# Optimization experiments

Hardware: AMD Instinct MI355X
Metric: run time of the kernel (lower is better)

## Reference

```python
import jax, jax.numpy as jnp
import numpy as np

B, N, D, K = 32, 4096, 128, 512
NPB = 2048          # unique tail nodes per batch (>= K so topk branch is taken)
M = B * NPB         # total unique tail nodes
E = B * N           # total edges
NUM_ENT = 10000


def setup_inputs() -> dict:
    key = jax.random.key(0)
    ks = jax.random.split(key, 18)
    f = lambda k, s: jax.random.normal(k, s, dtype=jnp.float32)
    inp = {
        "q_head": f(ks[0], (B, D)),
        "q_rel": f(ks[1], (B, D)),
        "q_time": f(ks[2], (B, D)),
        "r_neighbor": f(ks[3], (B, N, D)),
        "t_neighbor": f(ks[4], (B, N, D)),
        "time_neighbor": f(ks[5], (B, N, D)),
        "hidden": f(ks[6], (E, D)),
        "tail_emd": jnp.zeros((M, D), jnp.float32),  # scatter out-buffer
    }
    # tail_index: each edge of batch b scatters into that batch's node slab
    local = jax.random.randint(ks[7], (B, N), 0, NPB)
    inp["tail_index"] = (local + jnp.arange(B)[:, None] * NPB).reshape(E).astype(jnp.int32)
    # tail_nodes: [M,3] = (batch id, tail entity, time)
    batch_col = jnp.repeat(jnp.arange(B), NPB)
    tail_col = jax.random.randint(ks[8], (M,), 0, NUM_ENT)
    time_col = jax.random.randint(ks[9], (M,), 0, 365)
    inp["tail_nodes"] = jnp.stack([batch_col, tail_col, time_col], axis=-1).astype(jnp.int32)
    # linear-layer params (torch nn.Linear-style scaling)
    s3, s1 = 1.0 / np.sqrt(3 * D), 1.0 / np.sqrt(D)
    inp["W_q"] = f(ks[10], (3 * D, D)) * s3
    inp["b_q"] = jnp.zeros((D,), jnp.float32)
    inp["W_a"] = f(ks[11], (3 * D, D)) * s3
    inp["b_a"] = jnp.zeros((D,), jnp.float32)
    inp["W_att"] = f(ks[12], (3 * D, 1)) * s3
    inp["b_att"] = jnp.zeros((1,), jnp.float32)
    inp["W_rule"] = f(ks[13], (D, 1)) * s1
    inp["b_rule"] = jnp.zeros((1,), jnp.float32)
    inp["W_out"] = f(ks[14], (D, D)) * s1
    inp["b_out"] = jnp.zeros((D,), jnp.float32)
    return inp


def reference(q_head, q_rel, q_time, r_neighbor, t_neighbor, time_neighbor,
              hidden, tail_emd, tail_index, tail_nodes,
              W_q, b_q, W_a, b_a, W_att, b_att, W_rule, b_rule, W_out, b_out):
    # act = identity (module default). reduce = 'sum'.
    # raw message per edge: [E, D]
    message = (q_head[:, None, :] + r_neighbor + time_neighbor).reshape(E, D)
    # query / neighbor projections
    query = jnp.concatenate([q_head, q_rel, q_time], axis=-1) @ W_q + b_q      # [B, D]
    neigh = jnp.concatenate([r_neighbor, t_neighbor, time_neighbor], -1) @ W_a + b_a  # [B, N, D]
    q = query[:, None, :]
    qa = jnp.concatenate([q * neigh, q - neigh, q + neigh], axis=-1)           # [B, N, 3D]
    att1 = jax.nn.sigmoid(qa @ W_att + b_att).reshape(E, 1)
    att2 = jax.nn.sigmoid(hidden @ W_rule + b_rule)                            # [E, 1]
    att = (att1 + att2) * 0.5
    msg = att * message
    # scatter-sum aggregation over unique tail nodes
    seg = lambda v: jax.ops.segment_sum(v, tail_index, num_segments=M)
    tail_agg = tail_emd + seg(msg)            # scatter(..., out=tail_emd)
    new_hidden = seg(hidden)                  # [M, D]
    agg_att = seg(att[:, 0])                  # [M]
    # per-batch top-k over aggregated attention (each batch has NPB >= K nodes)
    nodes_batch = tail_nodes[:, 0]
    scores = jnp.where(nodes_batch[None, :] == jnp.arange(B)[:, None],
                       agg_att[None, :], -jnp.inf)                             # [B, M]
    _, idx = jax.lax.top_k(scores, K)                                          # [B, K] global node ids
    new_nodes = jnp.stack([tail_nodes[:, 1][idx], tail_nodes[:, 2][idx]], -1)  # [B, K, 2]
    emd = tail_agg[idx]                                                        # [B, K, D]
    hid = new_hidden[idx]                                                      # [B, K, D]
    out_emd = emd @ W_out + b_out                                              # act=identity
    return new_nodes, out_emd, hid
```

## Files before the change

### kernel.cpp

```cpp
#include <hip/hip_runtime.h>
#include <math.h>

#define B 32
#define N 4096
#define D 128
#define KTOP 512
#define NPB 2048
#define MSEG (B * NPB)
#define E (B * N)
#define MAXC 32

__global__ __launch_bounds__(128) void k0_precompute(
    const float* __restrict__ qh, const float* __restrict__ qr,
    const float* __restrict__ qt, const float* __restrict__ Wq,
    const float* __restrict__ bq, const float* __restrict__ Wa,
    const float* __restrict__ ba, const float* __restrict__ Watt,
    const float* __restrict__ batt, double* __restrict__ vws,
    double* __restrict__ c2ws, float* __restrict__ vf,
    float* __restrict__ c2f) {
  int b = blockIdx.x, d = threadIdx.x;
  __shared__ double u[128];
  __shared__ double red[128];
  const float* qhb = qh + b * 128;
  const float* qrb = qr + b * 128;
  const float* qtb = qt + b * 128;
  double acc = (double)bq[d];
  for (int i = 0; i < 128; ++i) acc += (double)qhb[i] * (double)Wq[i * 128 + d];
  for (int i = 0; i < 128; ++i) acc += (double)qrb[i] * (double)Wq[(128 + i) * 128 + d];
  for (int i = 0; i < 128; ++i) acc += (double)qtb[i] * (double)Wq[(256 + i) * 128 + d];
  double w1 = (double)Watt[d], w2 = (double)Watt[128 + d], w3 = (double)Watt[256 + d];
  double ud = acc * w1 - w2 + w3;
  u[d] = ud;
  red[d] = acc * (w2 + w3) + (double)ba[d] * ud;
  __syncthreads();
  for (int s = 64; s > 0; s >>= 1) {
    if (d < s) red[d] += red[d + s];
    __syncthreads();
  }
  if (d == 0) {
    double c2 = red[0] + (double)batt[0];
    c2ws[b] = c2;
    c2f[b] = (float)c2;
  }
  for (int i = d; i < 384; i += 128) {
    double vv = 0.0;
    for (int dd = 0; dd < 128; ++dd) vv += (double)Wa[i * 128 + dd] * u[dd];
    vws[b * 384 + i] = vv;
    vf[b * 384 + i] = (float)vv;
  }
}

__global__ __launch_bounds__(256) void k1_att(
    const float* __restrict__ r, const float* __restrict__ t,
    const float* __restrict__ tm, const float* __restrict__ hidden,
    const float* __restrict__ Wrule, const float* __restrict__ brule,
    const float* __restrict__ vf, const float* __restrict__ c2f,
    float* __restrict__ attw) {
  int tid = threadIdx.x;
  int h = tid >> 5;
  int l = tid & 31;
  int base = blockIdx.x * 64;
  int b = base >> 12;
  const float4* vb = (const float4*)(vf + b * 384);
  float4 v0 = vb[l];
  float4 v1 = vb[32 + l];
  float4 v2 = vb[64 + l];
  float4 wr = ((const float4*)Wrule)[l];
  float c2 = c2f[b];
  float br = brule[0];
#pragma unroll 4
  for (int i = 0; i < 8; ++i) {
    int e = base + i * 8 + h;
    size_t eo = (size_t)e * 128 + l * 4;
    float4 ra = *(const float4*)(r + eo);
    float4 ta = *(const float4*)(t + eo);
    float4 ma = *(const float4*)(tm + eo);
    float4 ha = *(const float4*)(hidden + eo);
    float p1 = ra.x * v0.x + ra.y * v0.y + ra.z * v0.z + ra.w * v0.w;
    p1 += ta.x * v1.x + ta.y * v1.y + ta.z * v1.z + ta.w * v1.w;
    p1 += ma.x * v2.x + ma.y * v2.y + ma.z * v2.z + ma.w * v2.w;
    float p2 = ha.x * wr.x + ha.y * wr.y + ha.z * wr.z + ha.w * wr.w;
#pragma unroll
    for (int off = 16; off > 0; off >>= 1) {
      p1 += __shfl_xor(p1, off);
      p2 += __shfl_xor(p2, off);
    }
    if (l == 0) {
      float a1 = 1.0f / (1.0f + expf(-(p1 + c2)));
      float a2 = 1.0f / (1.0f + expf(-(p2 + br)));
      attw[e] = 0.5f * (a1 + a2);
    }
  }
}

__global__ __launch_bounds__(256) void kb_build(const int* __restrict__ tidx,
                                                int* __restrict__ counts,
                                                int* __restrict__ lists) {
  int e = blockIdx.x * 256 + threadIdx.x;
  int m = tidx[e];
  int pos = atomicAdd(&counts[m], 1);
  if (pos < MAXC) lists[m * MAXC + pos] = e;
}

__global__ __launch_bounds__(256) void k_agg(const int* __restrict__ counts,
                                             const int* __restrict__ lists,
                                             const float* __restrict__ attw,
                                             float* __restrict__ agg_att) {
  int m = blockIdx.x * 256 + threadIdx.x;
  int cnt = counts[m];
  if (cnt > MAXC) cnt = MAXC;
  float s = 0.f;
  for (int j = 0; j < cnt; ++j) s += attw[lists[m * MAXC + j]];
  agg_att[m] = s;
}

__global__ __launch_bounds__(256) void k6_topk(
    const float* __restrict__ agg_att, const int* __restrict__ tail_nodes,
    float* __restrict__ out_nodes, int* __restrict__ idxw) {
  __shared__ float sv[2048];
  int b = blockIdx.x >> 3;
  int chunk = blockIdx.x & 7;
  int tid = threadIdx.x;
  for (int s = tid; s < 2048; s += 256) sv[s] = agg_att[b * 2048 + s];
  __syncthreads();
  int i = chunk * 256 + tid;
  float vi = sv[i];
  int rank = 0;
#pragma unroll 8
  for (int j = 0; j < 2048; ++j) {
    float vj = sv[j];
    rank += (vj > vi) || (vj == vi && j < i);
  }
  if (rank < KTOP) {
    int gm = b * 2048 + i;
    int p = b * KTOP + rank;
    out_nodes[p * 2 + 0] = (float)tail_nodes[gm * 3 + 1];
    out_nodes[p * 2 + 1] = (float)tail_nodes[gm * 3 + 2];
    idxw[p] = gm;
  }
}

__global__ __launch_bounds__(256) void k7_out(
    const float* __restrict__ tail_emd, const float* __restrict__ r,
    const float* __restrict__ tm, const float* __restrict__ hidden,
    const float* __restrict__ qh, const float* __restrict__ attw,
    const int* __restrict__ counts, const int* __restrict__ lists,
    const float* __restrict__ Wout, const float* __restrict__ bout,
    const int* __restrict__ idxw, float* __restrict__ out_emd,
    float* __restrict__ out_hid) {
  __shared__ float Ws[16384];
  __shared__ float es[256];
  int tid = threadIdx.x;
  int sub = tid >> 7, d = tid & 127;
  for (int i = tid; i < 16384; i += 256) Ws[i] = Wout[i];
  int base = blockIdx.x * 32;
  float bo = bout[d];
  for (int j = 0; j < 32; j += 2) {
    int row = base + j + sub;
    int m = idxw[row];
    int b = m >> 11;
    int cnt = counts[m];
    if (cnt > MAXC) cnt = MAXC;
    float accT = tail_emd[(size_t)m * 128 + d];
    float accH = 0.f;
    float qhd = qh[b * 128 + d];
    for (int jj = 0; jj < cnt; ++jj) {
      int e = lists[m * MAXC + jj];
      float a = attw[e];
      size_t eo = (size_t)e * 128 + d;
      accT += a * (qhd + r[eo] + tm[eo]);
      accH += hidden[eo];
    }
    __syncthreads();
    es[sub * 128 + d] = accT;
    __syncthreads();
    float acc = bo;
#pragma unroll 8
    for (int i = 0; i < 128; ++i) acc += es[sub * 128 + i] * Ws[i * 128 + d];
    out_emd[(size_t)row * 128 + d] = acc;
    out_hid[(size_t)row * 128 + d] = accH;
  }
}

extern "C" void kernel_launch(void* const* d_in, const int* in_sizes, int n_in,
                              void* d_out, int out_size, void* d_ws,
                              size_t ws_size, hipStream_t stream) {
  const float* q_head = (const float*)d_in[0];
  const float* q_rel = (const float*)d_in[1];
  const float* q_time = (const float*)d_in[2];
  const float* r_nb = (const float*)d_in[3];
  const float* t_nb = (const float*)d_in[4];
  const float* tm_nb = (const float*)d_in[5];
  const float* hidden = (const float*)d_in[6];
  const float* tail_emd = (const float*)d_in[7];
  const int* tail_index = (const int*)d_in[8];
  const int* tail_nodes = (const int*)d_in[9];
  const float* W_q = (const float*)d_in[10];
  const float* b_q = (const float*)d_in[11];
  const float* W_a = (const float*)d_in[12];
  const float* b_a = (const float*)d_in[13];
  const float* W_att = (const float*)d_in[14];
  const float* b_att = (const float*)d_in[15];
  const float* W_rule = (const float*)d_in[16];
  const float* b_rule = (const float*)d_in[17];
  const float* W_out = (const float*)d_in[18];
  const float* b_out = (const float*)d_in[19];

  char* ws = (char*)d_ws;
  double* vws = (double*)(ws + 0);
  double* c2ws = (double*)(ws + 98304);
  float* vf = (float*)(ws + 98560);
  float* c2f = (float*)(ws + 147712);
  float* attw = (float*)(ws + 147968);
  int* counts = (int*)(ws + 672256);
  int* lists = (int*)(ws + 934400);
  float* agg_att = (float*)(ws + 9323008);
  int* idxw = (int*)(ws + 9585152);

  float* out_nodes = (float*)d_out;
  float* out_emd = (float*)d_out + (size_t)B * KTOP * 2;
  float* out_hid = out_emd + (size_t)B * KTOP * 128;

  hipMemsetAsync(counts, 0, MSEG * sizeof(int), stream);
  k0_precompute<<<B, 128, 0, stream>>>(q_head, q_rel, q_time, W_q, b_q, W_a,
                                       b_a, W_att, b_att, vws, c2ws, vf, c2f);
  k1_att<<<E / 64, 256, 0, stream>>>(r_nb, t_nb, tm_nb, hidden, W_rule, b_rule,
                                     vf, c2f, attw);
  kb_build<<<E / 256, 256, 0, stream>>>(tail_index, counts, lists);
  k_agg<<<MSEG / 256, 256, 0, stream>>>(counts, lists, attw, agg_att);
  k6_topk<<<B * 8, 256, 0, stream>>>(agg_att, tail_nodes, out_nodes, idxw);
  k7_out<<<(B * KTOP) / 32, 256, 0, stream>>>(tail_emd, r_nb, tm_nb, hidden,
                                              q_head, attw, counts, lists,
                                              W_out, b_out, idxw, out_emd,
                                              out_hid);
}
```

Before: 501.3 us.

## Fuse attention aggregation into att kernel and restructure output projection

Attention aggregation moves into the attention kernel as double-precision atomics, which removes the separate aggregation kernel; top-k now ranks on doubles. The output kernel stops staging the full W_out in shared memory, handles 16 rows per block, and does a register-blocked float4 matmul after gathering rows, giving more blocks. The precompute kernel splits its serial double accumulations into four chains and drops unused double outputs. The trade-offs are atomic contention, an extra memset, and a double-width shared array in top-k.

```diff
diff --git a/kernel.cpp b/kernel.cpp
--- a/kernel.cpp
+++ b/kernel.cpp
@@ -9,14 +9,14 @@
 #define MSEG (B * NPB)
 #define E (B * N)
 #define MAXC 32
+#define K7ROWS 16
 
 __global__ __launch_bounds__(128) void k0_precompute(
     const float* __restrict__ qh, const float* __restrict__ qr,
     const float* __restrict__ qt, const float* __restrict__ Wq,
     const float* __restrict__ bq, const float* __restrict__ Wa,
     const float* __restrict__ ba, const float* __restrict__ Watt,
-    const float* __restrict__ batt, double* __restrict__ vws,
-    double* __restrict__ c2ws, float* __restrict__ vf,
+    const float* __restrict__ batt, float* __restrict__ vf,
     float* __restrict__ c2f) {
   int b = blockIdx.x, d = threadIdx.x;
   __shared__ double u[128];
@@ -24,10 +24,29 @@
   const float* qhb = qh + b * 128;
   const float* qrb = qr + b * 128;
   const float* qtb = qt + b * 128;
-  double acc = (double)bq[d];
-  for (int i = 0; i < 128; ++i) acc += (double)qhb[i] * (double)Wq[i * 128 + d];
-  for (int i = 0; i < 128; ++i) acc += (double)qrb[i] * (double)Wq[(128 + i) * 128 + d];
-  for (int i = 0; i < 128; ++i) acc += (double)qtb[i] * (double)Wq[(256 + i) * 128 + d];
+  double a0 = 0, a1 = 0, a2 = 0, a3 = 0;
+#pragma unroll 4
+  for (int i = 0; i < 128; i += 4) {
+    a0 += (double)qhb[i] * (double)Wq[i * 128 + d];
+    a1 += (double)qhb[i + 1] * (double)Wq[(i + 1) * 128 + d];
+    a2 += (double)qhb[i + 2] * (double)Wq[(i + 2) * 128 + d];
+    a3 += (double)qhb[i + 3] * (double)Wq[(i + 3) * 128 + d];
+  }
+#pragma unroll 4
+  for (int i = 0; i < 128; i += 4) {
+    a0 += (double)qrb[i] * (double)Wq[(128 + i) * 128 + d];
+    a1 += (double)qrb[i + 1] * (double)Wq[(129 + i) * 128 + d];
+    a2 += (double)qrb[i + 2] * (double)Wq[(130 + i) * 128 + d];
+    a3 += (double)qrb[i + 3] * (double)Wq[(131 + i) * 128 + d];
+  }
+#pragma unroll 4
+  for (int i = 0; i < 128; i += 4) {
+    a0 += (double)qtb[i] * (double)Wq[(256 + i) * 128 + d];
+    a1 += (double)qtb[i + 1] * (double)Wq[(257 + i) * 128 + d];
+    a2 += (double)qtb[i + 2] * (double)Wq[(258 + i) * 128 + d];
+    a3 += (double)qtb[i + 3] * (double)Wq[(259 + i) * 128 + d];
+  }
+  double acc = (double)bq[d] + ((a0 + a1) + (a2 + a3));
   double w1 = (double)Watt[d], w2 = (double)Watt[128 + d], w3 = (double)Watt[256 + d];
   double ud = acc * w1 - w2 + w3;
   u[d] = ud;
@@ -37,16 +56,17 @@
     if (d < s) red[d] += red[d + s];
     __syncthreads();
   }
-  if (d == 0) {
-    double c2 = red[0] + (double)batt[0];
-    c2ws[b] = c2;
-    c2f[b] = (float)c2;
-  }
+  if (d == 0) c2f[b] = (float)(red[0] + (double)batt[0]);
   for (int i = d; i < 384; i += 128) {
-    double vv = 0.0;
-    for (int dd = 0; dd < 128; ++dd) vv += (double)Wa[i * 128 + dd] * u[dd];
-    vws[b * 384 + i] = vv;
-    vf[b * 384 + i] = (float)vv;
+    double v0 = 0, v1 = 0, v2 = 0, v3 = 0;
+#pragma unroll 4
+    for (int dd = 0; dd < 128; dd += 4) {
+      v0 += (double)Wa[i * 128 + dd] * u[dd];
+      v1 += (double)Wa[i * 128 + dd + 1] * u[dd + 1];
+      v2 += (double)Wa[i * 128 + dd + 2] * u[dd + 2];
+      v3 += (double)Wa[i * 128 + dd + 3] * u[dd + 3];
+    }
+    vf[b * 384 + i] = (float)((v0 + v1) + (v2 + v3));
   }
 }
 
@@ -55,7 +75,8 @@
     const float* __restrict__ tm, const float* __restrict__ hidden,
     const float* __restrict__ Wrule, const float* __restrict__ brule,
     const float* __restrict__ vf, const float* __restrict__ c2f,
-    float* __restrict__ attw) {
+    const int* __restrict__ tidx, float* __restrict__ attw,
+    double* __restrict__ aggd) {
   int tid = threadIdx.x;
   int h = tid >> 5;
   int l = tid & 31;
@@ -88,7 +109,9 @@
     if (l == 0) {
       float a1 = 1.0f / (1.0f + expf(-(p1 + c2)));
       float a2 = 1.0f / (1.0f + expf(-(p2 + br)));
-      attw[e] = 0.5f * (a1 + a2);
+      float a = 0.5f * (a1 + a2);
+      attw[e] = a;
+      atomicAdd(&aggd[tidx[e]], (double)a);
     }
   }
 }
@@ -102,33 +125,21 @@
   if (pos < MAXC) lists[m * MAXC + pos] = e;
 }
 
-__global__ __launch_bounds__(256) void k_agg(const int* __restrict__ counts,
-                                             const int* __restrict__ lists,
-                                             const float* __restrict__ attw,
-                                             float* __restrict__ agg_att) {
-  int m = blockIdx.x * 256 + threadIdx.x;
-  int cnt = counts[m];
-  if (cnt > MAXC) cnt = MAXC;
-  float s = 0.f;
-  for (int j = 0; j < cnt; ++j) s += attw[lists[m * MAXC + j]];
-  agg_att[m] = s;
-}
-
 __global__ __launch_bounds__(256) void k6_topk(
-    const float* __restrict__ agg_att, const int* __restrict__ tail_nodes,
+    const double* __restrict__ aggd, const int* __restrict__ tail_nodes,
     float* __restrict__ out_nodes, int* __restrict__ idxw) {
-  __shared__ float sv[2048];
+  __shared__ double sv[2048];
   int b = blockIdx.x >> 3;
   int chunk = blockIdx.x & 7;
   int tid = threadIdx.x;
-  for (int s = tid; s < 2048; s += 256) sv[s] = agg_att[b * 2048 + s];
+  for (int s = tid; s < 2048; s += 256) sv[s] = aggd[b * 2048 + s];
   __syncthreads();
   int i = chunk * 256 + tid;
-  float vi = sv[i];
+  double vi = sv[i];
   int rank = 0;
 #pragma unroll 8
   for (int j = 0; j < 2048; ++j) {
-    float vj = sv[j];
+    double vj = sv[j];
     rank += (vj > vi) || (vj == vi && j < i);
   }
   if (rank < KTOP) {
@@ -148,14 +159,11 @@
     const float* __restrict__ Wout, const float* __restrict__ bout,
     const int* __restrict__ idxw, float* __restrict__ out_emd,
     float* __restrict__ out_hid) {
-  __shared__ float Ws[16384];
-  __shared__ float es[256];
+  __shared__ float es[K7ROWS][128];
   int tid = threadIdx.x;
   int sub = tid >> 7, d = tid & 127;
-  for (int i = tid; i < 16384; i += 256) Ws[i] = Wout[i];
-  int base = blockIdx.x * 32;
-  float bo = bout[d];
-  for (int j = 0; j < 32; j += 2) {
+  int base = blockIdx.x * K7ROWS;
+  for (int j = 0; j < K7ROWS; j += 2) {
     int row = base + j + sub;
     int m = idxw[row];
     int b = m >> 11;
@@ -171,15 +179,26 @@
       accT += a * (qhd + r[eo] + tm[eo]);
       accH += hidden[eo];
     }
-    __syncthreads();
-    es[sub * 128 + d] = accT;
-    __syncthreads();
-    float acc = bo;
-#pragma unroll 8
-    for (int i = 0; i < 128; ++i) acc += es[sub * 128 + i] * Ws[i * 128 + d];
-    out_emd[(size_t)row * 128 + d] = acc;
+    es[j + sub][d] = accT;
     out_hid[(size_t)row * 128 + d] = accH;
   }
+  __syncthreads();
+  int cg = tid & 31;
+  int rg = tid >> 5;
+  float4 bo = *(const float4*)(bout + cg * 4);
+  float acc0x = bo.x, acc0y = bo.y, acc0z = bo.z, acc0w = bo.w;
+  float acc1x = bo.x, acc1y = bo.y, acc1z = bo.z, acc1w = bo.w;
+#pragma unroll 4
+  for (int i = 0; i < 128; ++i) {
+    float4 w = *(const float4*)(Wout + i * 128 + cg * 4);
+    float e0 = es[rg * 2 + 0][i];
+    float e1 = es[rg * 2 + 1][i];
+    acc0x += e0 * w.x; acc0y += e0 * w.y; acc0z += e0 * w.z; acc0w += e0 * w.w;
+    acc1x += e1 * w.x; acc1y += e1 * w.y; acc1z += e1 * w.z; acc1w += e1 * w.w;
+  }
+  size_t r0 = (size_t)(base + rg * 2) * 128 + cg * 4;
+  *(float4*)(out_emd + r0) = make_float4(acc0x, acc0y, acc0z, acc0w);
+  *(float4*)(out_emd + r0 + 128) = make_float4(acc1x, acc1y, acc1z, acc1w);
 }
 
 extern "C" void kernel_launch(void* const* d_in, const int* in_sizes, int n_in,
@@ -207,30 +226,28 @@
   const float* b_out = (const float*)d_in[19];
 
   char* ws = (char*)d_ws;
-  double* vws = (double*)(ws + 0);
-  double* c2ws = (double*)(ws + 98304);
-  float* vf = (float*)(ws + 98560);
-  float* c2f = (float*)(ws + 147712);
-  float* attw = (float*)(ws + 147968);
-  int* counts = (int*)(ws + 672256);
-  int* lists = (int*)(ws + 934400);
-  float* agg_att = (float*)(ws + 9323008);
-  int* idxw = (int*)(ws + 9585152);
+  float* vf = (float*)(ws + 0);
+  float* c2f = (float*)(ws + 49152);
+  float* attw = (float*)(ws + 49280);
+  int* counts = (int*)(ws + 573568);
+  int* lists = (int*)(ws + 835712);
+  double* aggd = (double*)(ws + 9224320);
+  int* idxw = (int*)(ws + 9748608);
 
   float* out_nodes = (float*)d_out;
   float* out_emd = (float*)d_out + (size_t)B * KTOP * 2;
   float* out_hid = out_emd + (size_t)B * KTOP * 128;
 
   hipMemsetAsync(counts, 0, MSEG * sizeof(int), stream);
+  hipMemsetAsync(aggd, 0, MSEG * sizeof(double), stream);
   k0_precompute<<<B, 128, 0, stream>>>(q_head, q_rel, q_time, W_q, b_q, W_a,
-                                       b_a, W_att, b_att, vws, c2ws, vf, c2f);
+                                       b_a, W_att, b_att, vf, c2f);
   k1_att<<<E / 64, 256, 0, stream>>>(r_nb, t_nb, tm_nb, hidden, W_rule, b_rule,
-                                     vf, c2f, attw);
+                                     vf, c2f, tail_index, attw, aggd);
   kb_build<<<E / 256, 256, 0, stream>>>(tail_index, counts, lists);
-  k_agg<<<MSEG / 256, 256, 0, stream>>>(counts, lists, attw, agg_att);
-  k6_topk<<<B * 8, 256, 0, stream>>>(agg_att, tail_nodes, out_nodes, idxw);
-  k7_out<<<(B * KTOP) / 32, 256, 0, stream>>>(tail_emd, r_nb, tm_nb, hidden,
-                                              q_head, attw, counts, lists,
-                                              W_out, b_out, idxw, out_emd,
-                                              out_hid);
-}
+  k6_topk<<<B * 8, 256, 0, stream>>>(aggd, tail_nodes, out_nodes, idxw);
+  k7_out<<<(B * KTOP) / K7ROWS, 256, 0, stream>>>(tail_emd, r_nb, tm_nb,
+                                                  hidden, q_head, attw, counts,
+                                                  lists, W_out, b_out, idxw,
+                                                  out_emd, out_hid);
+}
```

Measured after the change: 461.9 us. 1.09x faster.
